# Optimization experiments

Measured on AMD Instinct MI355X. Metric: run time of the kernel, lower is better.

## Reference

```python
import jax, jax.numpy as jnp
import numpy as np

N = 50000      # nodes
E = 1_600_000  # edges
F_IN = 128; HID = 128; LAT = 64; OUT = 128; GEN = 2


def gcn_conv(x, src, dst, norm, W, b, n_nodes):
    """PyG GCNConv with self-loops already appended to (src, dst) and
    symmetric normalization `norm` precomputed per edge."""
    h = x @ W                                    # [N, out]
    msg = h[src] * norm[:, None]                 # [E+N, out] gather + scale
    out = jax.ops.segment_sum(msg, dst, num_segments=n_nodes)
    return out + b


def _self_loop_norm(edge_index, n_nodes):
    loops = jnp.arange(n_nodes, dtype=edge_index.dtype)
    src = jnp.concatenate([edge_index[0], loops])
    dst = jnp.concatenate([edge_index[1], loops])
    deg = jnp.zeros((n_nodes,), jnp.float32).at[dst].add(1.0)
    dinv = jnp.where(deg > 0, deg ** -0.5, 0.0)
    norm = dinv[src] * dinv[dst]
    return src, dst, norm


def setup_inputs() -> dict:
    key = jax.random.key(0)
    ks = jax.random.split(key, 12)
    p = lambda k, s: jax.random.normal(k, s, jnp.float32) * 0.05
    return {
        "x": jax.random.normal(ks[0], (N, F_IN), jnp.float32),
        "edge_index": jax.random.randint(ks[1], (2, E), 0, N, jnp.int32),
        "eps": jax.random.normal(ks[2], (N, LAT), jnp.float32),
        "u": jax.random.uniform(ks[3], (N, GEN), jnp.float32),
        "W1": p(ks[4], (F_IN, HID)), "b1": jnp.zeros((HID,), jnp.float32),
        "W_mu": p(ks[5], (HID, LAT)), "b_mu": jnp.zeros((LAT,), jnp.float32),
        "W_ls": p(ks[6], (HID, LAT)), "b_ls": jnp.zeros((LAT,), jnp.float32),
        "W_dx": p(ks[7], (LAT, OUT)), "b_dx": jnp.zeros((OUT,), jnp.float32),
        "W_g": p(ks[8], (LAT, GEN)), "b_g": jnp.zeros((GEN,), jnp.float32),
        "W_lc": p(ks[9], (LAT, 1)), "b_lc": jnp.zeros((1,), jnp.float32),
    }


def reference(x, edge_index, eps, u, W1, b1, W_mu, b_mu, W_ls, b_ls,
              W_dx, b_dx, W_g, b_g, W_lc, b_lc):
    n = x.shape[0]
    src, dst, norm = _self_loop_norm(edge_index, n)

    # Encoder: GCN -> relu -> (mu, logvar)
    h = jax.nn.relu(gcn_conv(x, src, dst, norm, W1, b1, n))
    mu = gcn_conv(h, src, dst, norm, W_mu, b_mu, n)
    logvar = gcn_conv(h, src, dst, norm, W_ls, b_ls, n)

    # reparameterize: z = eps * exp(0.5*logvar) + mu
    z = eps * jnp.exp(0.5 * logvar) + mu

    # decoders / classifiers
    recon_x = gcn_conv(z, src, dst, norm, W_dx, b_dx, n)
    logits_gender = gcn_conv(z, src, dst, norm, W_g, b_g, n)
    logits_label = z @ W_lc + b_lc

    # Gumbel-softmax (hard, straight-through), temperature=1.0
    g = -jnp.log(-jnp.log(u + 1e-20) + 1e-20)
    y_soft = jax.nn.softmax(logits_gender + g, axis=-1)
    y_hard = jax.nn.one_hot(jnp.argmax(y_soft, axis=-1), GEN, dtype=y_soft.dtype)
    gender = jax.lax.stop_gradient(y_hard - y_soft) + y_soft

    return (recon_x, gender, logits_label, mu, logvar, z)
```

## Files before the change

kernel.cpp:

```cpp
#include <hip/hip_runtime.h>
#include <hip/hip_fp16.h>
#include <cstddef>


constexpr int R = 200;
constexpr int NBUCK = 250;
constexpr int NBLK = 250;
constexpr int SLABCAP = 12288;

__global__ __launch_bounds__(256) void hist_kernel(
    const int* __restrict__ dst, int* __restrict__ gh, int e, int chunk) {
  __shared__ int h[NBUCK];
  for (int t = threadIdx.x; t < NBUCK; t += 256) h[t] = 0;
  __syncthreads();
  int beg = blockIdx.x * chunk;
  int fin = min(e, beg + chunk);
  for (int i = beg + threadIdx.x; i < fin; i += 256)
    atomicAdd(&h[dst[i] / R], 1);
  __syncthreads();
  for (int t = threadIdx.x; t < NBUCK; t += 256)
    gh[t * NBLK + blockIdx.x] = h[t];
}

__global__ void scan_p1(const int* __restrict__ in, int* __restrict__ part, int n) {
  __shared__ int s[256];
  int i = blockIdx.x * 256 + threadIdx.x;
  s[threadIdx.x] = (i < n) ? in[i] : 0;
  __syncthreads();
  for (int off = 128; off > 0; off >>= 1) {
    if (threadIdx.x < off) s[threadIdx.x] += s[threadIdx.x + off];
    __syncthreads();
  }
  if (threadIdx.x == 0) part[blockIdx.x] = s[0];
}

__global__ void scan_p2(int* __restrict__ part, int nb, int* __restrict__ total_out) {
  __shared__ int s[256];
  int v = (threadIdx.x < nb) ? part[threadIdx.x] : 0;
  s[threadIdx.x] = v;
  __syncthreads();
  for (int off = 1; off < 256; off <<= 1) {
    int t = (threadIdx.x >= off) ? s[threadIdx.x - off] : 0;
    __syncthreads();
    s[threadIdx.x] += t;
    __syncthreads();
  }
  if (threadIdx.x < nb) part[threadIdx.x] = s[threadIdx.x] - v;
  if (threadIdx.x == nb - 1) *total_out = s[threadIdx.x];
}

__global__ void scan_p3(int* io, const int* __restrict__ part, int n) {
  __shared__ int s[256];
  int i = blockIdx.x * 256 + threadIdx.x;
  int v = (i < n) ? io[i] : 0;
  s[threadIdx.x] = v;
  __syncthreads();
  for (int off = 1; off < 256; off <<= 1) {
    int t = (threadIdx.x >= off) ? s[threadIdx.x - off] : 0;
    __syncthreads();
    s[threadIdx.x] += t;
    __syncthreads();
  }
  int excl = s[threadIdx.x] - v + part[blockIdx.x];
  if (i < n) io[i] = excl;
}

__global__ __launch_bounds__(256) void scatter_kernel(
    const int* __restrict__ src, const int* __restrict__ dst,
    const int* __restrict__ ghs, int* __restrict__ binned, int e, int chunk) {
  __shared__ int cur[NBUCK];
  for (int t = threadIdx.x; t < NBUCK; t += 256)
    cur[t] = ghs[t * NBLK + blockIdx.x];
  __syncthreads();
  int beg = blockIdx.x * chunk;
  int fin = min(e, beg + chunk);
  for (int i = beg + threadIdx.x; i < fin; i += 256) {
    int d = dst[i];
    int b = d / R;
    int p = atomicAdd(&cur[b], 1);
    binned[p] = ((d - b * R) << 16) | src[i];
  }
}

__global__ __launch_bounds__(256) void final_kernel(
    const int* __restrict__ binned, const int* __restrict__ ghs,
    int* __restrict__ rowptr, int* __restrict__ csr,
    float* __restrict__ dinv, int n, int e) {
  __shared__ int sdeg[R];
  __shared__ int sscan[256];
  __shared__ int scur[R];
  __shared__ int slab[SLABCAP];
  const int b = blockIdx.x;
  const int tid = threadIdx.x;
  const int base = ghs[b * NBLK];
  const int end = (b < NBUCK - 1) ? ghs[(b + 1) * NBLK] : e;
  const int cnt = end - base;

  if (tid < R) sdeg[tid] = 0;
  __syncthreads();
  for (int k = base + tid; k < end; k += 256)
    atomicAdd(&sdeg[binned[k] >> 16], 1);
  __syncthreads();

  int dv = (tid < R) ? sdeg[tid] : 0;
  sscan[tid] = dv;
  __syncthreads();
  for (int off = 1; off < 256; off <<= 1) {
    int t = (tid >= off) ? sscan[tid - off] : 0;
    __syncthreads();
    sscan[tid] += t;
    __syncthreads();
  }
  int excl = sscan[tid] - dv;
  int node = b * R + tid;
  if (tid < R && node < n) {
    rowptr[node] = base + excl;
    dinv[node] = 1.0f / sqrtf((float)dv + 1.0f);
    scur[tid] = excl;
  }
  __syncthreads();

  const bool fits = (cnt <= SLABCAP);
  for (int k = base + tid; k < end; k += 256) {
    int rec = binned[k];
    int p = atomicAdd(&scur[rec >> 16], 1);
    int s = rec & 0xFFFF;
    if (fits) slab[p] = s;
    else csr[base + p] = s;
  }
  __syncthreads();
  if (fits)
    for (int k = tid; k < cnt; k += 256) csr[base + k] = slab[k];
}

template <int K, int M, int KT, int RPT, bool BIAS, bool RELU, bool HALF_OUT>
__global__ __launch_bounds__(256, 4) void gemm_kernel(
    const float* __restrict__ A, const float* __restrict__ W,
    const float* __restrict__ bias, float* __restrict__ C,
    __half* __restrict__ Ch, const float* __restrict__ dinv, int n) {
  constexpr int CG = M / 4;
  constexpr int RS = 256 / CG;
  constexpr int RPB = RS * RPT;
  __shared__ float sW[KT * M];
  const int cg = threadIdx.x % CG;
  const int rs = threadIdx.x / CG;
  const int row0 = blockIdx.x * RPB + rs * RPT;

  const float* Arow[RPT];
#pragma unroll
  for (int rr = 0; rr < RPT; ++rr) {
    int row = row0 + rr;
    if (row > n - 1) row = n - 1;
    Arow[rr] = A + (size_t)row * K;
  }

  float4 acc[RPT];
#pragma unroll
  for (int rr = 0; rr < RPT; ++rr) acc[rr] = float4{0.f, 0.f, 0.f, 0.f};

  for (int kt = 0; kt < K; kt += KT) {
    if (kt) __syncthreads();
    for (int i = threadIdx.x * 4; i < KT * M; i += 1024)
      *reinterpret_cast<float4*>(&sW[i]) =
          *reinterpret_cast<const float4*>(&W[kt * M + i]);
    __syncthreads();
#pragma unroll 4
    for (int k4 = 0; k4 < KT; k4 += 4) {
      float4 a[RPT];
#pragma unroll
      for (int rr = 0; rr < RPT; ++rr)
        a[rr] = *reinterpret_cast<const float4*>(Arow[rr] + kt + k4);
#pragma unroll
      for (int j = 0; j < 4; ++j) {
        float4 w = *reinterpret_cast<const float4*>(&sW[(k4 + j) * M + cg * 4]);
#pragma unroll
        for (int rr = 0; rr < RPT; ++rr) {
          float av = reinterpret_cast<const float*>(&a[rr])[j];
          acc[rr].x += av * w.x;
          acc[rr].y += av * w.y;
          acc[rr].z += av * w.z;
          acc[rr].w += av * w.w;
        }
      }
    }
  }

  float4 bv = float4{0.f, 0.f, 0.f, 0.f};
  if (BIAS) bv = *reinterpret_cast<const float4*>(&bias[cg * 4]);
#pragma unroll
  for (int rr = 0; rr < RPT; ++rr) {
    int row = row0 + rr;
    if (row < n) {
      float4 o = acc[rr];
      if (BIAS) { o.x += bv.x; o.y += bv.y; o.z += bv.z; o.w += bv.w; }
      if (RELU) {
        o.x = fmaxf(o.x, 0.f); o.y = fmaxf(o.y, 0.f);
        o.z = fmaxf(o.z, 0.f); o.w = fmaxf(o.w, 0.f);
      }
      if (HALF_OUT) {
        float di = dinv[row];
        __half2* dst = reinterpret_cast<__half2*>(Ch + (size_t)row * M + cg * 4);
        dst[0] = __floats2half2_rn(di * o.x, di * o.y);
        dst[1] = __floats2half2_rn(di * o.z, di * o.w);
      } else {
        *reinterpret_cast<float4*>(&C[(size_t)row * M + cg * 4]) = o;
      }
    }
  }
}

template <int F, bool BIAS, bool RELU, bool HALF_OUT>
__global__ __launch_bounds__(256) void spmm_kernel(
    const __half* __restrict__ Xs, void* __restrict__ Yout,
    const int* __restrict__ rowptr, const int* __restrict__ csr,
    const float* __restrict__ dinv, const float* __restrict__ bias, int n) {
  int wid = (blockIdx.x * blockDim.x + threadIdx.x) >> 6;
  int lane = threadIdx.x & 63;
  if (wid >= n) return;
  int beg = rowptr[wid];
  int end = rowptr[wid + 1];
  constexpr int V = F / 64;
  constexpr int U = 8;
  float acc0[U], acc1[U];
#pragma unroll
  for (int uu = 0; uu < U; ++uu) { acc0[uu] = 0.f; acc1[uu] = 0.f; }

  for (int base = beg; base < end; base += 64) {
    int m = end - base;
    if (m > 64) m = 64;
    int idx = (lane < m) ? csr[base + lane] : 0;
    int j = 0;
    for (; j + U <= m; j += U) {
      const __half* rows[U];
#pragma unroll
      for (int uu = 0; uu < U; ++uu)
        rows[uu] = Xs + (size_t)__shfl(idx, j + uu, 64) * F;
      if (V == 2) {
        __half2 v[U];
#pragma unroll
        for (int uu = 0; uu < U; ++uu)
          v[uu] = reinterpret_cast<const __half2*>(rows[uu])[lane];
#pragma unroll
        for (int uu = 0; uu < U; ++uu) {
          float2 f = __half22float2(v[uu]);
          acc0[uu] += f.x;
          acc1[uu] += f.y;
        }
      } else {
        __half v[U];
#pragma unroll
        for (int uu = 0; uu < U; ++uu) v[uu] = rows[uu][lane];
#pragma unroll
        for (int uu = 0; uu < U; ++uu) acc0[uu] += __half2float(v[uu]);
      }
    }
    for (; j < m; ++j) {
      const __half* row = Xs + (size_t)__shfl(idx, j, 64) * F;
      if (V == 2) {
        float2 f = __half22float2(reinterpret_cast<const __half2*>(row)[lane]);
        acc0[0] += f.x;
        acc1[0] += f.y;
      } else {
        acc0[0] += __half2float(row[lane]);
      }
    }
  }

  float t0 = 0.f, t1 = 0.f;
#pragma unroll
  for (int uu = 0; uu < U; ++uu) { t0 += acc0[uu]; t1 += acc1[uu]; }

  const __half* srow = Xs + (size_t)wid * F;
  if (V == 2) {
    float2 sf = __half22float2(reinterpret_cast<const __half2*>(srow)[lane]);
    t0 += sf.x;
    t1 += sf.y;
  } else {
    t0 += __half2float(srow[lane]);
  }

  float di = dinv[wid];
  float r0 = di * t0;
  float r1 = di * t1;
  if (BIAS) {
    if (V == 2) { r0 += bias[lane * 2]; r1 += bias[lane * 2 + 1]; }
    else r0 += bias[lane];
  }
  if (RELU) { r0 = fmaxf(r0, 0.f); r1 = fmaxf(r1, 0.f); }

  if (HALF_OUT) {
    __half* Yh = (__half*)Yout;
    if (V == 2)
      reinterpret_cast<__half2*>(Yh + (size_t)wid * F)[lane] =
          __floats2half2_rn(di * r0, di * r1);
    else
      Yh[(size_t)wid * F + lane] = __float2half(di * r0);
  } else {
    float* Yf = (float*)Yout;
    if (V == 2) {
      float2 o = {r0, r1};
      reinterpret_cast<float2*>(Yf + (size_t)wid * F)[lane] = o;
    } else {
      Yf[(size_t)wid * F + lane] = r0;
    }
  }
}

__global__ void z_kernel(const float* __restrict__ eps, const float* __restrict__ lv,
                         const float* __restrict__ mu, float* __restrict__ z,
                         __half* __restrict__ zh, const float* __restrict__ dinv,
                         int n64) {
  int i = blockIdx.x * blockDim.x + threadIdx.x;
  if (i < n64) {
    float zv = eps[i] * expf(0.5f * lv[i]) + mu[i];
    z[i] = zv;
    zh[i] = __float2half(dinv[i >> 6] * zv);
  }
}

__global__ __launch_bounds__(256) void zg_kernel(
    const float* __restrict__ z, const float* __restrict__ Wg,
    const float* __restrict__ Wlc, const float* __restrict__ blc,
    const float* __restrict__ dinv, float2* __restrict__ zgs,
    float* __restrict__ out_label, int n) {
  int wid = (blockIdx.x * blockDim.x + threadIdx.x) >> 6;
  int lane = threadIdx.x & 63;
  if (wid >= n) return;
  float zz = z[(size_t)wid * 64 + lane];
  float v0 = zz * Wg[lane * 2 + 0];
  float v1 = zz * Wg[lane * 2 + 1];
  float v2 = zz * Wlc[lane];
  for (int off = 32; off > 0; off >>= 1) {
    v0 += __shfl_xor(v0, off, 64);
    v1 += __shfl_xor(v1, off, 64);
    v2 += __shfl_xor(v2, off, 64);
  }
  if (lane == 0) {
    float di = dinv[wid];
    zgs[wid] = float2{di * v0, di * v1};
    out_label[wid] = v2 + blc[0];
  }
}

__global__ __launch_bounds__(256) void gagg_kernel(
    const float2* __restrict__ zgs, const int* __restrict__ rowptr,
    const int* __restrict__ csr, const float* __restrict__ dinv,
    const float* __restrict__ bg, const float* __restrict__ u,
    float* __restrict__ out_gender, int n) {
  int wid = (blockIdx.x * blockDim.x + threadIdx.x) >> 6;
  int lane = threadIdx.x & 63;
  if (wid >= n) return;
  int beg = rowptr[wid];
  int end = rowptr[wid + 1];
  float a0 = 0.f, a1 = 0.f;
  for (int k = beg + lane; k < end; k += 64) {
    float2 g = zgs[csr[k]];
    a0 += g.x;
    a1 += g.y;
  }
  for (int off = 32; off > 0; off >>= 1) {
    a0 += __shfl_xor(a0, off, 64);
    a1 += __shfl_xor(a1, off, 64);
  }
  if (lane == 0) {
    float2 self = zgs[wid];
    a0 += self.x;
    a1 += self.y;
    float di = dinv[wid];
    float lg0 = di * a0 + bg[0];
    float lg1 = di * a1 + bg[1];
    float u0 = u[(size_t)wid * 2 + 0];
    float u1 = u[(size_t)wid * 2 + 1];
    float g0 = -logf(-logf(u0 + 1e-20f) + 1e-20f);
    float g1 = -logf(-logf(u1 + 1e-20f) + 1e-20f);
    float aa0 = lg0 + g0, aa1 = lg1 + g1;
    float mx = fmaxf(aa0, aa1);
    float e0 = expf(aa0 - mx), e1 = expf(aa1 - mx);
    float s = e0 + e1;
    float y0 = e0 / s, y1 = e1 / s;
    float h0 = (y1 > y0) ? 0.f : 1.f;
    float h1 = 1.f - h0;
    out_gender[(size_t)wid * 2 + 0] = (h0 - y0) + y0;
    out_gender[(size_t)wid * 2 + 1] = (h1 - y1) + y1;
  }
}

extern "C" void kernel_launch(void* const* d_in, const int* in_sizes, int n_in,
                              void* d_out, int out_size, void* d_ws, size_t ws_size,
                              hipStream_t stream) {
  const float* x   = (const float*)d_in[0];
  const int*   ei  = (const int*)d_in[1];
  const float* eps = (const float*)d_in[2];
  const float* u   = (const float*)d_in[3];
  const float* W1  = (const float*)d_in[4];
  const float* b1  = (const float*)d_in[5];
  const float* Wmu = (const float*)d_in[6];
  const float* bmu = (const float*)d_in[7];
  const float* Wls = (const float*)d_in[8];
  const float* bls = (const float*)d_in[9];
  const float* Wdx = (const float*)d_in[10];
  const float* bdx = (const float*)d_in[11];
  const float* Wg  = (const float*)d_in[12];
  const float* bg  = (const float*)d_in[13];
  const float* Wlc = (const float*)d_in[14];
  const float* blc = (const float*)d_in[15];

  const int n = in_sizes[0] / 128;
  const int e = in_sizes[1] / 2;
  const int* esrc = ei;
  const int* edst = ei + e;

  float* out = (float*)d_out;
  float* out_recon  = out;
  float* out_gender = out + (size_t)n * 128;
  float* out_label  = out_gender + (size_t)n * 2;
  float* out_mu     = out_label + n;
  float* out_lv     = out_mu + (size_t)n * 64;
  float* out_z      = out_lv + (size_t)n * 64;

  float* dinv  = (float*)d_ws;
  int* rowptr  = (int*)(dinv + n);
  int* part    = rowptr + (n + 1);
  int* csr     = part + 256;
  int* gh      = csr + e;
  __half* Xs   = (__half*)(gh + NBUCK * NBLK);
  __half* hb   = Xs + (size_t)n * 128;
  float* zgs   = (float*)(hb + (size_t)n * 128);
  __half* zh   = Xs;
  float* zagg  = (float*)hb;
  float* hagg  = out_recon;
  int* binned  = (int*)out_lv;

  const int GH = NBUCK * NBLK;
  const int GHB = (GH + 255) / 256;
  const int chunk = (e + NBLK - 1) / NBLK;

  hist_kernel<<<NBLK, 256, 0, stream>>>(edst, gh, e, chunk);
  scan_p1<<<GHB, 256, 0, stream>>>(gh, part, GH);
  scan_p2<<<1, 256, 0, stream>>>(part, GHB, &rowptr[n]);
  scan_p3<<<GHB, 256, 0, stream>>>(gh, part, GH);
  scatter_kernel<<<NBLK, 256, 0, stream>>>(esrc, edst, gh, binned, e, chunk);
  final_kernel<<<NBUCK, 256, 0, stream>>>(binned, gh, rowptr, csr, dinv, n, e);

  gemm_kernel<128, 128, 64, 4, false, false, true>
      <<<(n + 31) / 32, 256, 0, stream>>>(x, W1, nullptr, nullptr, Xs, dinv, n);
  spmm_kernel<128, true, true, true>
      <<<(n + 3) / 4, 256, 0, stream>>>(Xs, hb, rowptr, csr, dinv, b1, n);
  spmm_kernel<128, false, false, false>
      <<<(n + 3) / 4, 256, 0, stream>>>(hb, hagg, rowptr, csr, dinv, nullptr, n);
  gemm_kernel<128, 64, 64, 4, true, false, false>
      <<<(n + 63) / 64, 256, 0, stream>>>(hagg, Wmu, bmu, out_mu, nullptr, nullptr, n);
  gemm_kernel<128, 64, 64, 4, true, false, false>
      <<<(n + 63) / 64, 256, 0, stream>>>(hagg, Wls, bls, out_lv, nullptr, nullptr, n);
  z_kernel<<<(n * 64 + 255) / 256, 256, 0, stream>>>(eps, out_lv, out_mu, out_z, zh, dinv, n * 64);
  zg_kernel<<<(n + 3) / 4, 256, 0, stream>>>(out_z, Wg, Wlc, blc, dinv, (float2*)zgs, out_label, n);
  spmm_kernel<64, false, false, false>
      <<<(n + 3) / 4, 256, 0, stream>>>(zh, zagg, rowptr, csr, dinv, nullptr, n);
  gemm_kernel<64, 128, 64, 4, true, false, false>
      <<<(n + 31) / 32, 256, 0, stream>>>(zagg, Wdx, bdx, out_recon, nullptr, nullptr, n);
  gagg_kernel<<<(n + 3) / 4, 256, 0, stream>>>((const float2*)zgs, rowptr, csr, dinv, bg, u, out_gender, n);
}
```

Measured before the change: 487.5 us.

## Fuse mu/logvar GEMMs with reparameterization and merge z aggregation with gender aggregation

Combines the two 128x64 GEMMs, the z reparameterization, and the gender/label projections into a single kernel that reads hagg once and writes mu, logvar, z, a scaled z copy and the per-node gender/label partials. The scaled z used for the decoder aggregation is now stored in fp8 instead of fp16, which halves its gather traffic. The 64-wide SpMM is merged with the gender aggregation so that each neighbor list is walked only once. This removes several kernel launches and intermediate round trips, but fp8 quantization of z reduces the accuracy of recon_x.

```diff
diff --git a/kernel.cpp b/kernel.cpp
--- a/kernel.cpp
+++ b/kernel.cpp
@@ -209,8 +209,8 @@
   }
 }
 
-template <int F, bool BIAS, bool RELU, bool HALF_OUT>
-__global__ __launch_bounds__(256) void spmm_kernel(
+template <bool BIAS, bool RELU, bool HALF_OUT>
+__global__ __launch_bounds__(256) void spmm128_kernel(
     const __half* __restrict__ Xs, void* __restrict__ Yout,
     const int* __restrict__ rowptr, const int* __restrict__ csr,
     const float* __restrict__ dinv, const float* __restrict__ bias, int n) {
@@ -219,11 +219,10 @@
   if (wid >= n) return;
   int beg = rowptr[wid];
   int end = rowptr[wid + 1];
-  constexpr int V = F / 64;
   constexpr int U = 8;
-  float acc0[U], acc1[U];
-#pragma unroll
-  for (int uu = 0; uu < U; ++uu) { acc0[uu] = 0.f; acc1[uu] = 0.f; }
+  float a0[U], a1[U];
+#pragma unroll
+  for (int uu = 0; uu < U; ++uu) { a0[uu] = 0.f; a1[uu] = 0.f; }
 
   for (int base = beg; base < end; base += 64) {
     int m = end - base;
@@ -231,119 +230,172 @@
     int idx = (lane < m) ? csr[base + lane] : 0;
     int j = 0;
     for (; j + U <= m; j += U) {
-      const __half* rows[U];
+      const __half2* rows[U];
 #pragma unroll
       for (int uu = 0; uu < U; ++uu)
-        rows[uu] = Xs + (size_t)__shfl(idx, j + uu, 64) * F;
-      if (V == 2) {
-        __half2 v[U];
-#pragma unroll
-        for (int uu = 0; uu < U; ++uu)
-          v[uu] = reinterpret_cast<const __half2*>(rows[uu])[lane];
-#pragma unroll
-        for (int uu = 0; uu < U; ++uu) {
-          float2 f = __half22float2(v[uu]);
-          acc0[uu] += f.x;
-          acc1[uu] += f.y;
-        }
-      } else {
-        __half v[U];
-#pragma unroll
-        for (int uu = 0; uu < U; ++uu) v[uu] = rows[uu][lane];
-#pragma unroll
-        for (int uu = 0; uu < U; ++uu) acc0[uu] += __half2float(v[uu]);
+        rows[uu] = reinterpret_cast<const __half2*>(
+            Xs + (size_t)__shfl(idx, j + uu, 64) * 128);
+      __half2 v[U];
+#pragma unroll
+      for (int uu = 0; uu < U; ++uu) v[uu] = rows[uu][lane];
+#pragma unroll
+      for (int uu = 0; uu < U; ++uu) {
+        float2 f = __half22float2(v[uu]);
+        a0[uu] += f.x;
+        a1[uu] += f.y;
       }
     }
     for (; j < m; ++j) {
-      const __half* row = Xs + (size_t)__shfl(idx, j, 64) * F;
-      if (V == 2) {
-        float2 f = __half22float2(reinterpret_cast<const __half2*>(row)[lane]);
-        acc0[0] += f.x;
-        acc1[0] += f.y;
-      } else {
-        acc0[0] += __half2float(row[lane]);
-      }
+      const __half2* row = reinterpret_cast<const __half2*>(
+          Xs + (size_t)__shfl(idx, j, 64) * 128);
+      float2 f = __half22float2(row[lane]);
+      a0[0] += f.x;
+      a1[0] += f.y;
     }
   }
 
   float t0 = 0.f, t1 = 0.f;
 #pragma unroll
-  for (int uu = 0; uu < U; ++uu) { t0 += acc0[uu]; t1 += acc1[uu]; }
-
-  const __half* srow = Xs + (size_t)wid * F;
-  if (V == 2) {
-    float2 sf = __half22float2(reinterpret_cast<const __half2*>(srow)[lane]);
-    t0 += sf.x;
-    t1 += sf.y;
-  } else {
-    t0 += __half2float(srow[lane]);
-  }
+  for (int uu = 0; uu < U; ++uu) { t0 += a0[uu]; t1 += a1[uu]; }
+
+  float2 sf = __half22float2(
+      reinterpret_cast<const __half2*>(Xs + (size_t)wid * 128)[lane]);
+  t0 += sf.x;
+  t1 += sf.y;
 
   float di = dinv[wid];
   float r0 = di * t0;
   float r1 = di * t1;
-  if (BIAS) {
-    if (V == 2) { r0 += bias[lane * 2]; r1 += bias[lane * 2 + 1]; }
-    else r0 += bias[lane];
-  }
+  if (BIAS) { r0 += bias[lane * 2]; r1 += bias[lane * 2 + 1]; }
   if (RELU) { r0 = fmaxf(r0, 0.f); r1 = fmaxf(r1, 0.f); }
 
   if (HALF_OUT) {
-    __half* Yh = (__half*)Yout;
-    if (V == 2)
-      reinterpret_cast<__half2*>(Yh + (size_t)wid * F)[lane] =
-          __floats2half2_rn(di * r0, di * r1);
-    else
-      Yh[(size_t)wid * F + lane] = __float2half(di * r0);
+    reinterpret_cast<__half2*>((__half*)Yout + (size_t)wid * 128)[lane] =
+        __floats2half2_rn(di * r0, di * r1);
   } else {
-    float* Yf = (float*)Yout;
-    if (V == 2) {
-      float2 o = {r0, r1};
-      reinterpret_cast<float2*>(Yf + (size_t)wid * F)[lane] = o;
-    } else {
-      Yf[(size_t)wid * F + lane] = r0;
-    }
-  }
-}
-
-__global__ void z_kernel(const float* __restrict__ eps, const float* __restrict__ lv,
-                         const float* __restrict__ mu, float* __restrict__ z,
-                         __half* __restrict__ zh, const float* __restrict__ dinv,
-                         int n64) {
-  int i = blockIdx.x * blockDim.x + threadIdx.x;
-  if (i < n64) {
-    float zv = eps[i] * expf(0.5f * lv[i]) + mu[i];
-    z[i] = zv;
-    zh[i] = __float2half(dinv[i >> 6] * zv);
-  }
-}
-
-__global__ __launch_bounds__(256) void zg_kernel(
-    const float* __restrict__ z, const float* __restrict__ Wg,
-    const float* __restrict__ Wlc, const float* __restrict__ blc,
-    const float* __restrict__ dinv, float2* __restrict__ zgs,
-    float* __restrict__ out_label, int n) {
-  int wid = (blockIdx.x * blockDim.x + threadIdx.x) >> 6;
-  int lane = threadIdx.x & 63;
-  if (wid >= n) return;
-  float zz = z[(size_t)wid * 64 + lane];
-  float v0 = zz * Wg[lane * 2 + 0];
-  float v1 = zz * Wg[lane * 2 + 1];
-  float v2 = zz * Wlc[lane];
-  for (int off = 32; off > 0; off >>= 1) {
-    v0 += __shfl_xor(v0, off, 64);
-    v1 += __shfl_xor(v1, off, 64);
-    v2 += __shfl_xor(v2, off, 64);
-  }
-  if (lane == 0) {
-    float di = dinv[wid];
-    zgs[wid] = float2{di * v0, di * v1};
-    out_label[wid] = v2 + blc[0];
-  }
-}
-
-__global__ __launch_bounds__(256) void gagg_kernel(
-    const float2* __restrict__ zgs, const int* __restrict__ rowptr,
+    float2 o = {r0, r1};
+    reinterpret_cast<float2*>((float*)Yout + (size_t)wid * 128)[lane] = o;
+  }
+}
+
+__global__ __launch_bounds__(256, 4) void mlz_kernel(
+    const float* __restrict__ hagg,
+    const float* __restrict__ Wmu, const float* __restrict__ bmu,
+    const float* __restrict__ Wls, const float* __restrict__ bls,
+    const float* __restrict__ eps, const float* __restrict__ dinv,
+    const float* __restrict__ Wg, const float* __restrict__ Wlc,
+    const float* __restrict__ blc,
+    float* __restrict__ out_mu, float* __restrict__ out_lv,
+    float* __restrict__ out_z, unsigned int* __restrict__ zh8,
+    float2* __restrict__ zgs, float* __restrict__ out_label, int n) {
+  constexpr int K = 128, M = 64, KT = 64, RPT = 4;
+  constexpr int CG = M / 4;
+  constexpr int RS = 256 / CG;
+  constexpr int RPB = RS * RPT;
+  __shared__ float sWm[KT * M];
+  __shared__ float sWl[KT * M];
+  const int cg = threadIdx.x % CG;
+  const int rs = threadIdx.x / CG;
+  const int row0 = blockIdx.x * RPB + rs * RPT;
+
+  const float* Arow[RPT];
+#pragma unroll
+  for (int rr = 0; rr < RPT; ++rr) {
+    int row = row0 + rr;
+    if (row > n - 1) row = n - 1;
+    Arow[rr] = hagg + (size_t)row * K;
+  }
+
+  float4 am[RPT], al[RPT];
+#pragma unroll
+  for (int rr = 0; rr < RPT; ++rr) {
+    am[rr] = float4{0.f, 0.f, 0.f, 0.f};
+    al[rr] = float4{0.f, 0.f, 0.f, 0.f};
+  }
+
+  for (int kt = 0; kt < K; kt += KT) {
+    if (kt) __syncthreads();
+    for (int i = threadIdx.x * 4; i < KT * M; i += 1024) {
+      *reinterpret_cast<float4*>(&sWm[i]) =
+          *reinterpret_cast<const float4*>(&Wmu[kt * M + i]);
+      *reinterpret_cast<float4*>(&sWl[i]) =
+          *reinterpret_cast<const float4*>(&Wls[kt * M + i]);
+    }
+    __syncthreads();
+#pragma unroll 2
+    for (int k4 = 0; k4 < KT; k4 += 4) {
+      float4 a[RPT];
+#pragma unroll
+      for (int rr = 0; rr < RPT; ++rr)
+        a[rr] = *reinterpret_cast<const float4*>(Arow[rr] + kt + k4);
+#pragma unroll
+      for (int j = 0; j < 4; ++j) {
+        float4 wm = *reinterpret_cast<const float4*>(&sWm[(k4 + j) * M + cg * 4]);
+        float4 wl = *reinterpret_cast<const float4*>(&sWl[(k4 + j) * M + cg * 4]);
+#pragma unroll
+        for (int rr = 0; rr < RPT; ++rr) {
+          float av = reinterpret_cast<const float*>(&a[rr])[j];
+          am[rr].x += av * wm.x; am[rr].y += av * wm.y;
+          am[rr].z += av * wm.z; am[rr].w += av * wm.w;
+          al[rr].x += av * wl.x; al[rr].y += av * wl.y;
+          al[rr].z += av * wl.z; al[rr].w += av * wl.w;
+        }
+      }
+    }
+  }
+
+  float4 bm = *reinterpret_cast<const float4*>(&bmu[cg * 4]);
+  float4 bl = *reinterpret_cast<const float4*>(&bls[cg * 4]);
+  float wg0[4], wg1[4], wlcv[4];
+#pragma unroll
+  for (int cc = 0; cc < 4; ++cc) {
+    int c = cg * 4 + cc;
+    wg0[cc] = Wg[c * 2 + 0];
+    wg1[cc] = Wg[c * 2 + 1];
+    wlcv[cc] = Wlc[c];
+  }
+  float blc0 = blc[0];
+
+#pragma unroll
+  for (int rr = 0; rr < RPT; ++rr) {
+    int row = row0 + rr;
+    if (row < n) {
+      float4 mu4 = {am[rr].x + bm.x, am[rr].y + bm.y,
+                    am[rr].z + bm.z, am[rr].w + bm.w};
+      float4 lv4 = {al[rr].x + bl.x, al[rr].y + bl.y,
+                    al[rr].z + bl.z, al[rr].w + bl.w};
+      float4 e4 = *reinterpret_cast<const float4*>(&eps[(size_t)row * 64 + cg * 4]);
+      float4 z4 = {e4.x * expf(0.5f * lv4.x) + mu4.x,
+                   e4.y * expf(0.5f * lv4.y) + mu4.y,
+                   e4.z * expf(0.5f * lv4.z) + mu4.z,
+                   e4.w * expf(0.5f * lv4.w) + mu4.w};
+      *reinterpret_cast<float4*>(&out_mu[(size_t)row * 64 + cg * 4]) = mu4;
+      *reinterpret_cast<float4*>(&out_lv[(size_t)row * 64 + cg * 4]) = lv4;
+      *reinterpret_cast<float4*>(&out_z[(size_t)row * 64 + cg * 4]) = z4;
+      float di = dinv[row];
+      int pw = __builtin_amdgcn_cvt_pk_fp8_f32(di * z4.x, di * z4.y, 0, false);
+      pw = __builtin_amdgcn_cvt_pk_fp8_f32(di * z4.z, di * z4.w, pw, true);
+      zh8[(size_t)row * 16 + cg] = (unsigned int)pw;
+      float pg0 = z4.x * wg0[0] + z4.y * wg0[1] + z4.z * wg0[2] + z4.w * wg0[3];
+      float pg1 = z4.x * wg1[0] + z4.y * wg1[1] + z4.z * wg1[2] + z4.w * wg1[3];
+      float pl  = z4.x * wlcv[0] + z4.y * wlcv[1] + z4.z * wlcv[2] + z4.w * wlcv[3];
+#pragma unroll
+      for (int off = 1; off < 16; off <<= 1) {
+        pg0 += __shfl_xor(pg0, off, 64);
+        pg1 += __shfl_xor(pg1, off, 64);
+        pl  += __shfl_xor(pl, off, 64);
+      }
+      if (cg == 0) {
+        zgs[row] = float2{di * pg0, di * pg1};
+        out_label[row] = pl + blc0;
+      }
+    }
+  }
+}
+
+__global__ __launch_bounds__(256) void spmm_zg_kernel(
+    const unsigned char* __restrict__ zh8, const float2* __restrict__ zgs,
+    float* __restrict__ zagg, const int* __restrict__ rowptr,
     const int* __restrict__ csr, const float* __restrict__ dinv,
     const float* __restrict__ bg, const float* __restrict__ u,
     float* __restrict__ out_gender, int n) {
@@ -352,30 +404,66 @@
   if (wid >= n) return;
   int beg = rowptr[wid];
   int end = rowptr[wid + 1];
-  float a0 = 0.f, a1 = 0.f;
-  for (int k = beg + lane; k < end; k += 64) {
-    float2 g = zgs[csr[k]];
-    a0 += g.x;
-    a1 += g.y;
-  }
+  constexpr int U = 8;
+  float acc[U];
+#pragma unroll
+  for (int uu = 0; uu < U; ++uu) acc[uu] = 0.f;
+  float ga0 = 0.f, ga1 = 0.f;
+
+  for (int base = beg; base < end; base += 64) {
+    int m = end - base;
+    if (m > 64) m = 64;
+    int idx = 0;
+    if (lane < m) {
+      idx = csr[base + lane];
+      float2 g = zgs[idx];
+      ga0 += g.x;
+      ga1 += g.y;
+    }
+    int j = 0;
+    for (; j + U <= m; j += U) {
+      const unsigned char* rows[U];
+#pragma unroll
+      for (int uu = 0; uu < U; ++uu)
+        rows[uu] = zh8 + (size_t)__shfl(idx, j + uu, 64) * 64;
+      int b[U];
+#pragma unroll
+      for (int uu = 0; uu < U; ++uu) b[uu] = (int)rows[uu][lane];
+#pragma unroll
+      for (int uu = 0; uu < U; ++uu)
+        acc[uu] += __builtin_amdgcn_cvt_f32_fp8(b[uu], 0);
+    }
+    for (; j < m; ++j) {
+      const unsigned char* row = zh8 + (size_t)__shfl(idx, j, 64) * 64;
+      acc[0] += __builtin_amdgcn_cvt_f32_fp8((int)row[lane], 0);
+    }
+  }
+
+  float t = 0.f;
+#pragma unroll
+  for (int uu = 0; uu < U; ++uu) t += acc[uu];
+  t += __builtin_amdgcn_cvt_f32_fp8((int)zh8[(size_t)wid * 64 + lane], 0);
+
+  float di = dinv[wid];
+  zagg[(size_t)wid * 64 + lane] = di * t;
+
   for (int off = 32; off > 0; off >>= 1) {
-    a0 += __shfl_xor(a0, off, 64);
-    a1 += __shfl_xor(a1, off, 64);
+    ga0 += __shfl_xor(ga0, off, 64);
+    ga1 += __shfl_xor(ga1, off, 64);
   }
   if (lane == 0) {
     float2 self = zgs[wid];
-    a0 += self.x;
-    a1 += self.y;
-    float di = dinv[wid];
-    float lg0 = di * a0 + bg[0];
-    float lg1 = di * a1 + bg[1];
+    ga0 += self.x;
+    ga1 += self.y;
+    float lg0 = di * ga0 + bg[0];
+    float lg1 = di * ga1 + bg[1];
     float u0 = u[(size_t)wid * 2 + 0];
     float u1 = u[(size_t)wid * 2 + 1];
     float g0 = -logf(-logf(u0 + 1e-20f) + 1e-20f);
     float g1 = -logf(-logf(u1 + 1e-20f) + 1e-20f);
-    float aa0 = lg0 + g0, aa1 = lg1 + g1;
-    float mx = fmaxf(aa0, aa1);
-    float e0 = expf(aa0 - mx), e1 = expf(aa1 - mx);
+    float a0 = lg0 + g0, a1 = lg1 + g1;
+    float mx = fmaxf(a0, a1);
+    float e0 = expf(a0 - mx), e1 = expf(a1 - mx);
     float s = e0 + e1;
     float y0 = e0 / s, y1 = e1 / s;
     float h0 = (y1 > y0) ? 0.f : 1.f;
@@ -418,15 +506,22 @@
   float* out_lv     = out_mu + (size_t)n * 64;
   float* out_z      = out_lv + (size_t)n * 64;
 
-  float* dinv  = (float*)d_ws;
-  int* rowptr  = (int*)(dinv + n);
-  int* part    = rowptr + (n + 1);
-  int* csr     = part + 256;
-  int* gh      = csr + e;
-  __half* Xs   = (__half*)(gh + NBUCK * NBLK);
-  __half* hb   = Xs + (size_t)n * 128;
-  float* zgs   = (float*)(hb + (size_t)n * 128);
-  __half* zh   = Xs;
+  char* w = (char*)d_ws;
+  size_t off = 0;
+  auto alloc = [&](size_t bytes) {
+    char* p = w + off;
+    off = (off + bytes + 255) & ~(size_t)255;
+    return p;
+  };
+  float* dinv  = (float*)alloc((size_t)n * 4);
+  int* rowptr  = (int*)alloc((size_t)(n + 1) * 4);
+  int* part    = (int*)alloc(256 * 4);
+  int* csr     = (int*)alloc((size_t)e * 4);
+  int* gh      = (int*)alloc((size_t)NBUCK * NBLK * 4);
+  __half* Xs   = (__half*)alloc((size_t)n * 128 * 2);
+  __half* hb   = (__half*)alloc((size_t)n * 128 * 2);
+  float2* zgs  = (float2*)alloc((size_t)n * 8);
+  unsigned char* zh8 = (unsigned char*)Xs;
   float* zagg  = (float*)hb;
   float* hagg  = out_recon;
   int* binned  = (int*)out_lv;
@@ -444,19 +539,15 @@
 
   gemm_kernel<128, 128, 64, 4, false, false, true>
       <<<(n + 31) / 32, 256, 0, stream>>>(x, W1, nullptr, nullptr, Xs, dinv, n);
-  spmm_kernel<128, true, true, true>
+  spmm128_kernel<true, true, true>
       <<<(n + 3) / 4, 256, 0, stream>>>(Xs, hb, rowptr, csr, dinv, b1, n);
-  spmm_kernel<128, false, false, false>
+  spmm128_kernel<false, false, false>
       <<<(n + 3) / 4, 256, 0, stream>>>(hb, hagg, rowptr, csr, dinv, nullptr, n);
-  gemm_kernel<128, 64, 64, 4, true, false, false>
-      <<<(n + 63) / 64, 256, 0, stream>>>(hagg, Wmu, bmu, out_mu, nullptr, nullptr, n);
-  gemm_kernel<128, 64, 64, 4, true, false, false>
-      <<<(n + 63) / 64, 256, 0, stream>>>(hagg, Wls, bls, out_lv, nullptr, nullptr, n);
-  z_kernel<<<(n * 64 + 255) / 256, 256, 0, stream>>>(eps, out_lv, out_mu, out_z, zh, dinv, n * 64);
-  zg_kernel<<<(n + 3) / 4, 256, 0, stream>>>(out_z, Wg, Wlc, blc, dinv, (float2*)zgs, out_label, n);
-  spmm_kernel<64, false, false, false>
-      <<<(n + 3) / 4, 256, 0, stream>>>(zh, zagg, rowptr, csr, dinv, nullptr, n);
+  mlz_kernel<<<(n + 63) / 64, 256, 0, stream>>>(
+      hagg, Wmu, bmu, Wls, bls, eps, dinv, Wg, Wlc, blc,
+      out_mu, out_lv, out_z, (unsigned int*)zh8, zgs, out_label, n);
+  spmm_zg_kernel<<<(n + 3) / 4, 256, 0, stream>>>(
+      zh8, (const float2*)zgs, zagg, rowptr, csr, dinv, bg, u, out_gender, n);
   gemm_kernel<64, 128, 64, 4, true, false, false>
       <<<(n + 31) / 32, 256, 0, stream>>>(zagg, Wdx, bdx, out_recon, nullptr, nullptr, n);
-  gagg_kernel<<<(n + 3) / 4, 256, 0, stream>>>((const float2*)zgs, rowptr, csr, dinv, bg, u, out_gender, n);
-}
+}
```

Measured after the change: 416.6 us. -14.6%, faster.
